# Kernel optimization log

Measured on AMD Instinct MI355X. Metric: run time of the kernel, lower is better.

Reference implementation:

```python
import jax, jax.numpy as jnp
import numpy as np

# MANO kinematic tree (16 LBS joints): wrist root, 5 fingers x 3 joints
PARENTS = np.array([-1, 0, 1, 2, 0, 4, 5, 0, 7, 8, 0, 10, 11, 0, 13, 14])
B, NV, NJ_LBS, NJ_REG, NCOMPS = 4096, 1084, 16, 21, 45


def rodrigues(r):
    """Axis-angle [N,3] -> rotation matrices [N,3,3]."""
    eps = 1e-8
    angle = jnp.sqrt(jnp.sum(r * r, axis=-1, keepdims=True) + eps)  # [N,1]
    axis = r / angle
    c = jnp.cos(angle)[..., None]  # [N,1,1]
    s = jnp.sin(angle)[..., None]
    x, y, z = axis[:, 0], axis[:, 1], axis[:, 2]
    zeros = jnp.zeros_like(x)
    K = jnp.stack([zeros, -z, y, z, zeros, -x, -y, x, zeros], axis=-1).reshape(-1, 3, 3)
    I = jnp.eye(3, dtype=r.dtype)
    return I + s * K + (1.0 - c) * jnp.matmul(K, K)


def global_rigid_transform(Rs, Js):
    """Rs [B,16,3,3], Js [B,16,3] -> (posed joints [B,16,3], relative transforms A [B,16,4,4])."""
    b = Rs.shape[0]
    bottom = jnp.broadcast_to(jnp.array([0.0, 0.0, 0.0, 1.0], dtype=Rs.dtype), (b, 1, 4))

    def make_A(R, t):  # R [B,3,3], t [B,3] -> [B,4,4]
        top = jnp.concatenate([R, t[..., None]], axis=-1)
        return jnp.concatenate([top, bottom], axis=1)

    results = [make_A(Rs[:, 0], Js[:, 0])]
    for i in range(1, NJ_LBS):  # fixed small loop over kinematic tree
        p = int(PARENTS[i])
        t = Js[:, i] - Js[:, p]
        results.append(jnp.matmul(results[p], make_A(Rs[:, i], t)))
    A_world = jnp.stack(results, axis=1)  # [B,16,4,4]
    new_J = A_world[:, :, :3, 3]
    # A = A_world - pack(A_world @ [J;0])  (remove rest-pose joint translation)
    Jh = jnp.concatenate([Js, jnp.zeros_like(Js[..., :1])], axis=-1)  # [B,16,4]
    init_bone = jnp.einsum('bjpq,bjq->bjp', A_world, Jh)  # [B,16,4]
    A_rel = A_world.at[:, :, :, 3].add(-init_bone)
    return new_J, A_rel


def setup_inputs() -> dict:
    key = jax.random.key(0)
    ks = jax.random.split(key, 8)
    beta = jax.random.normal(ks[0], (B, 10), dtype=jnp.float32)
    theta = jax.random.normal(ks[1], (B, NCOMPS), dtype=jnp.float32)
    wrist_euler = jax.random.normal(ks[2], (B, 3), dtype=jnp.float32) * 0.3
    v_template = jax.random.normal(ks[3], (NV, 3), dtype=jnp.float32) * 0.1
    J_regressor = jax.nn.softmax(jax.random.normal(ks[4], (NV, NJ_REG), dtype=jnp.float32) * 4.0, axis=0)
    hands_comp = jax.random.normal(ks[5], (NCOMPS, 45), dtype=jnp.float32) * 0.05
    hands_mean = jax.random.normal(ks[6], (45,), dtype=jnp.float32) * 0.1
    weights = jax.nn.softmax(jax.random.normal(ks[7], (NV, NJ_LBS), dtype=jnp.float32) * 4.0, axis=1)
    return {"beta": beta, "theta": theta, "wrist_euler": wrist_euler,
            "v_template": v_template, "J_regressor": J_regressor,
            "hands_comp": hands_comp, "hands_mean": hands_mean, "weights": weights}


def reference(beta, theta, wrist_euler, v_template, J_regressor, hands_comp, hands_mean, weights):
    num_batch = beta.shape[0]  # beta only sets batch; forward ignores its values (as in source)
    # rest-pose joints from template: [21,3]
    Jt = jnp.einsum('vc,vj->jc', v_template, J_regressor)
    J = jnp.broadcast_to(Jt[None], (num_batch, NJ_REG, 3))
    # pose_type == 'pca'
    euler_pose = theta @ hands_comp + hands_mean  # [B,45]
    Rs = rodrigues(euler_pose.reshape(-1, 3)).reshape(num_batch, 15, 3, 3)
    global_rot = rodrigues(wrist_euler.reshape(-1, 3)).reshape(num_batch, 1, 3, 3)
    R_all = jnp.concatenate([global_rot, Rs], axis=1)  # [B,16,3,3]
    J_transformed, A = global_rigid_transform(R_all, J[:, :NJ_LBS])
    # linear blend skinning: T = W @ A  -> [B,Nv,4,4]
    W = jnp.broadcast_to(weights[None], (num_batch, NV, NJ_LBS))
    T = jnp.matmul(W, A.reshape(num_batch, NJ_LBS, 16)).reshape(num_batch, NV, 4, 4)
    vh = jnp.concatenate([v_template, jnp.ones_like(v_template[:, :1])], axis=-1)  # [Nv,4]
    verts = jnp.einsum('bvpq,vq->bvp', T, vh)[:, :, :3]  # [B,Nv,3]
    joints = jnp.einsum('bvc,vj->bjc', verts, J_regressor)  # [B,21,3]
    return verts, joints
```

## Files before the change

### kernel.cpp

```cpp
#include <hip/hip_runtime.h>

#define NV 1084
#define NVPAD 1088
#define NPART 64
#define NBATCH 8

typedef __attribute__((ext_vector_type(8))) short short8v;
typedef __attribute__((ext_vector_type(4))) float f32x4;

__device__ inline unsigned short f2bf(float f) {
    unsigned int u = __float_as_uint(f);
    unsigned int r = (u + 0x7FFFu + ((u >> 16) & 1u)) >> 16;
    return (unsigned short)r;
}


__device__ inline void rodrigues9(float x, float y, float z, float R[9]) {
    float n2 = x * x + y * y + z * z + 1e-8f;
    float angle = sqrtf(n2);
    float inv = 1.0f / angle;
    float ax = x * inv, ay = y * inv, az = z * inv;
    float c = cosf(angle), s = sinf(angle);
    float C = 1.0f - c;
    R[0] = 1.0f - C * (ay * ay + az * az);
    R[1] = -s * az + C * ax * ay;
    R[2] = s * ay + C * ax * az;
    R[3] = s * az + C * ax * ay;
    R[4] = 1.0f - C * (ax * ax + az * az);
    R[5] = -s * ax + C * ay * az;
    R[6] = -s * ay + C * ax * az;
    R[7] = s * ax + C * ay * az;
    R[8] = 1.0f - C * (ax * ax + ay * ay);
}

__global__ __launch_bounds__(384) void prep_kernel(
    const float* __restrict__ vt, const float* __restrict__ jreg,
    const float* __restrict__ wts, float* __restrict__ Mpart,
    unsigned short* __restrict__ Gbf) {
    int blk = blockIdx.x;
    int t = threadIdx.x;
    if (blk < NPART) {
        int p = blk;
        int v0 = p * 17, v1 = min(v0 + 17, NV);
        float* mp = Mpart + (size_t)p * 1392;
        if (t < 336) {
            int j = t >> 4, k = t & 15;
            float m0 = 0.f, m1 = 0.f, m2 = 0.f, s = 0.f;
            for (int v = v0; v < v1; ++v) {
                float jw = jreg[v * 21 + j] * wts[v * 16 + k];
                m0 += jw * vt[v * 3 + 0];
                m1 += jw * vt[v * 3 + 1];
                m2 += jw * vt[v * 3 + 2];
                s += jw;
            }
            mp[t * 4 + 0] = m0;
            mp[t * 4 + 1] = m1;
            mp[t * 4 + 2] = m2;
            mp[t * 4 + 3] = s;
        } else if (t < 384) {
            int o = t - 336;
            int j = o / 3, c = o - j * 3;
            float acc = 0.f;
            for (int v = v0; v < v1; ++v) acc += vt[v * 3 + c] * jreg[v * 21 + j];
            mp[1344 + o] = acc;
        }
    } else {
        int idx = (blk - NPART) * 384 + t;
        if (idx < NVPAD * 64) {
            int v = idx >> 6, i = idx & 63;
            int k = i >> 2, d = i & 3;
            float val = 0.f;
            if (v < NV) {
                float vh = (d == 3) ? 1.f : vt[v * 3 + d];
                val = wts[v * 16 + k] * vh;
            }
            Gbf[idx] = f2bf(val);
        }
    }
}

__global__ __launch_bounds__(256) void fk_kernel(
    const float* __restrict__ theta, const float* __restrict__ wrist,
    const float* __restrict__ hc, const float* __restrict__ hm,
    const float* __restrict__ Mpart, float* __restrict__ wsA,
    float* __restrict__ Mfinal, unsigned short* __restrict__ Abf,
    int total, int nFK) {
    int blk = blockIdx.x;
    int t = threadIdx.x;
    if (blk >= nFK) {
        __shared__ float sm[256];
        int q = (blk - nFK) * 64 + (t & 63);
        int pg = t >> 6;
        float acc = 0.f;
#pragma unroll
        for (int u = 0; u < 16; ++u) acc += Mpart[(size_t)(pg * 16 + u) * 1392 + q];
        sm[t] = acc;
        __syncthreads();
        if (pg == 0) Mfinal[q] = sm[t] + sm[t + 64] + sm[t + 128] + sm[t + 192];
        return;
    }
    __shared__ float sred[192];
    __shared__ float sj[48];
    if (t < 192) {
        int g = t / 48, o = t - g * 48;
        float acc = 0.f;
#pragma unroll
        for (int u = 0; u < 16; ++u)
            acc += Mpart[(size_t)(g * 16 + u) * 1392 + 1344 + o];
        sred[t] = acc;
    }
    __syncthreads();
    if (t < 48) sj[t] = sred[t] + sred[48 + t] + sred[96 + t] + sred[144 + t];
    __syncthreads();

    int idx = blk * 256 + t;
    if (idx >= total) return;
    int b = idx / 5, r = idx - b * 5;

    float e[9];
    {
        const float* th = theta + (size_t)b * 45;
        int base = 9 * r;
#pragma unroll
        for (int col = 0; col < 9; ++col) e[col] = hm[base + col];
        for (int k = 0; k < 45; ++k) {
            float tk = th[k];
            const float* hck = hc + k * 45 + base;
#pragma unroll
            for (int col = 0; col < 9; ++col) e[col] += tk * hck[col];
        }
    }

    float R[9];
    rodrigues9(wrist[b * 3 + 0], wrist[b * 3 + 1], wrist[b * 3 + 2], R);
    float J0x = sj[0], J0y = sj[1], J0z = sj[2];
    float Ap[12];
    Ap[0] = R[0]; Ap[1] = R[1]; Ap[2] = R[2]; Ap[3] = J0x;
    Ap[4] = R[3]; Ap[5] = R[4]; Ap[6] = R[5]; Ap[7] = J0y;
    Ap[8] = R[6]; Ap[9] = R[7]; Ap[10] = R[8]; Ap[11] = J0z;
    float* out = wsA + (size_t)b * 192;
    if (r == 0) {
#pragma unroll
        for (int row = 0; row < 3; ++row) {
            float a0 = Ap[row * 4 + 0], a1 = Ap[row * 4 + 1], a2 = Ap[row * 4 + 2];
            float a3 = Ap[row * 4 + 3] - (a0 * J0x + a1 * J0y + a2 * J0z);
            out[row * 4 + 0] = a0;
            out[row * 4 + 1] = a1;
            out[row * 4 + 2] = a2;
            out[row * 4 + 3] = a3;
            ushort4 h;
            h.x = f2bf(a0); h.y = f2bf(a1); h.z = f2bf(a2); h.w = f2bf(a3);
            *(ushort4*)(Abf + (size_t)(3 * b + row) * 64) = h;
        }
    }
    float px = J0x, py = J0y, pz = J0z;
#pragma unroll
    for (int s = 0; s < 3; ++s) {
        int i = r * 3 + s + 1;
        rodrigues9(e[3 * s + 0], e[3 * s + 1], e[3 * s + 2], R);
        float jx = sj[i * 3 + 0], jy = sj[i * 3 + 1], jz = sj[i * 3 + 2];
        float tx = jx - px, ty = jy - py, tz = jz - pz;
        float An[12];
#pragma unroll
        for (int row = 0; row < 3; ++row) {
            An[row * 4 + 0] = Ap[row * 4 + 0] * R[0] + Ap[row * 4 + 1] * R[3] + Ap[row * 4 + 2] * R[6];
            An[row * 4 + 1] = Ap[row * 4 + 0] * R[1] + Ap[row * 4 + 1] * R[4] + Ap[row * 4 + 2] * R[7];
            An[row * 4 + 2] = Ap[row * 4 + 0] * R[2] + Ap[row * 4 + 1] * R[5] + Ap[row * 4 + 2] * R[8];
            An[row * 4 + 3] = Ap[row * 4 + 3] + Ap[row * 4 + 0] * tx + Ap[row * 4 + 1] * ty + Ap[row * 4 + 2] * tz;
        }
        float* oi = out + i * 12;
#pragma unroll
        for (int row = 0; row < 3; ++row) {
            float a0 = An[row * 4 + 0], a1 = An[row * 4 + 1], a2 = An[row * 4 + 2];
            float a3 = An[row * 4 + 3] - (a0 * jx + a1 * jy + a2 * jz);
            oi[row * 4 + 0] = a0;
            oi[row * 4 + 1] = a1;
            oi[row * 4 + 2] = a2;
            oi[row * 4 + 3] = a3;
            ushort4 h;
            h.x = f2bf(a0); h.y = f2bf(a1); h.z = f2bf(a2); h.w = f2bf(a3);
            *(ushort4*)(Abf + (size_t)(3 * b + row) * 64 + 4 * i) = h;
        }
#pragma unroll
        for (int q = 0; q < 12; ++q) Ap[q] = An[q];
        px = jx; py = jy; pz = jz;
    }
}

#define SCW 1092
__global__ __launch_bounds__(256) void verts_joints_kernel(
    const float* __restrict__ wsA, const float* __restrict__ Mfinal,
    const unsigned short* __restrict__ Abf, const unsigned short* __restrict__ Gbf,
    float* __restrict__ verts, float* __restrict__ jout, int nVB) {
    int bid = blockIdx.x;
    int t = threadIdx.x;

    if (bid < nVB) {
        __shared__ float sC[12 * SCW];
        int b0 = bid * 4;
        int w = t >> 6, lane = t & 63;
        int lrow = lane & 15, lk = lane >> 4;

        const unsigned short* Ar = Abf + (size_t)(b0 * 3 + lrow) * 64 + lk * 8;
        short8v a0 = *(const short8v*)Ar;
        short8v a1 = *(const short8v*)(Ar + 32);

        for (int vt4 = w; vt4 < NVPAD / 16; vt4 += 4) {
            int v = vt4 * 16 + lrow;
            const unsigned short* Br = Gbf + (size_t)v * 64 + lk * 8;
            short8v g0 = *(const short8v*)Br;
            short8v g1 = *(const short8v*)(Br + 32);
            f32x4 acc = {0.f, 0.f, 0.f, 0.f};
            acc = __builtin_amdgcn_mfma_f32_16x16x32_bf16(a0, g0, acc, 0, 0, 0);
            acc = __builtin_amdgcn_mfma_f32_16x16x32_bf16(a1, g1, acc, 0, 0, 0);
            if (lk < 3) {
                float* dst = &sC[(lk * 4) * SCW + vt4 * 16 + lrow];
#pragma unroll
                for (int q = 0; q < 4; ++q) dst[q * SCW] = acc[q];
            }
        }
        __syncthreads();

        float* outp = verts + (size_t)b0 * (NV * 3);
#pragma unroll 1
        for (int f = t; f < 3252; f += 256) {
            int bl = f / 813;
            int off = (f - bl * 813) * 4;
            f32x4 val;
#pragma unroll
            for (int j = 0; j < 4; ++j) {
                int o = off + j;
                int v_ = o / 3, p_ = o - v_ * 3;
                val[j] = sC[(bl * 3 + p_) * SCW + v_];
            }
            __builtin_nontemporal_store(val, (f32x4*)(outp + (size_t)f * 4));
        }
    } else {
        int b0 = (bid - nVB) * NBATCH;
        for (int o = t; o < NBATCH * 63; o += 256) {
            int bl = o / 63;
            int rem = o - bl * 63;
            int j = rem / 3;
            int c = rem - j * 3;
            const float* A = wsA + (size_t)(b0 + bl) * 192 + c * 4;
            const float* Mj = Mfinal + j * 64;
            float acc = 0.f;
#pragma unroll
            for (int k = 0; k < 16; ++k) {
                float4 av = *(const float4*)&A[k * 12];
                float4 m = *(const float4*)&Mj[k * 4];
                acc += av.x * m.x + av.y * m.y + av.z * m.z + av.w * m.w;
            }
            __builtin_nontemporal_store(acc, jout + (size_t)(b0 + bl) * 63 + rem);
        }
    }
}

extern "C" void kernel_launch(void* const* d_in, const int* in_sizes, int n_in,
                              void* d_out, int out_size, void* d_ws, size_t ws_size,
                              hipStream_t stream) {
    const float* theta = (const float*)d_in[1];
    const float* wrist = (const float*)d_in[2];
    const float* vtpl  = (const float*)d_in[3];
    const float* jreg  = (const float*)d_in[4];
    const float* hc    = (const float*)d_in[5];
    const float* hm    = (const float*)d_in[6];
    const float* wts   = (const float*)d_in[7];
    int B = in_sizes[1] / 45;

    float* ws     = (float*)d_ws;
    float* wsA    = ws;
    float* Mpart  = ws + (size_t)B * 192;
    float* Mfinal = Mpart + (size_t)NPART * 1392;
    unsigned short* Gbf = (unsigned short*)(Mfinal + 1344);
    unsigned short* Abf = Gbf + (size_t)NVPAD * 64;
    float* verts  = (float*)d_out;
    float* jout   = verts + (size_t)B * NV * 3;

    int nG = (NVPAD * 64 + 383) / 384;
    prep_kernel<<<NPART + nG, 384, 0, stream>>>(vtpl, jreg, wts, Mpart, Gbf);
    int nFK = (B * 5 + 255) / 256;
    fk_kernel<<<nFK + 21, 256, 0, stream>>>(theta, wrist, hc, hm, Mpart, wsA,
                                            Mfinal, Abf, B * 5, nFK);
    int nVB = B / 4;
    verts_joints_kernel<<<nVB + B / NBATCH, 256, 0, stream>>>(
        wsA, Mfinal, Abf, Gbf, verts, jout, nVB);
}
```

Baseline: 51.84 us.

## Fuse prep and FK kernels, compute regressor reductions in-block instead of partials

After: 74.08 us. +42.9%, slower.

```diff
diff --git a/kernel.cpp b/kernel.cpp
--- a/kernel.cpp
+++ b/kernel.cpp
@@ -2,7 +2,6 @@
 
 #define NV 1084
 #define NVPAD 1088
-#define NPART 64
 #define NBATCH 8
 
 typedef __attribute__((ext_vector_type(8))) short short8v;
@@ -33,39 +32,18 @@
     R[8] = 1.0f - C * (ax * ax + ay * ay);
 }
 
-__global__ __launch_bounds__(384) void prep_kernel(
+__global__ __launch_bounds__(256) void prep_fk_kernel(
+    const float* __restrict__ theta, const float* __restrict__ wrist,
+    const float* __restrict__ hc, const float* __restrict__ hm,
     const float* __restrict__ vt, const float* __restrict__ jreg,
-    const float* __restrict__ wts, float* __restrict__ Mpart,
-    unsigned short* __restrict__ Gbf) {
+    const float* __restrict__ wts, float* __restrict__ wsA,
+    float* __restrict__ Mfinal, unsigned short* __restrict__ Gbf,
+    unsigned short* __restrict__ Abf, int total, int nFK) {
     int blk = blockIdx.x;
     int t = threadIdx.x;
-    if (blk < NPART) {
-        int p = blk;
-        int v0 = p * 17, v1 = min(v0 + 17, NV);
-        float* mp = Mpart + (size_t)p * 1392;
-        if (t < 336) {
-            int j = t >> 4, k = t & 15;
-            float m0 = 0.f, m1 = 0.f, m2 = 0.f, s = 0.f;
-            for (int v = v0; v < v1; ++v) {
-                float jw = jreg[v * 21 + j] * wts[v * 16 + k];
-                m0 += jw * vt[v * 3 + 0];
-                m1 += jw * vt[v * 3 + 1];
-                m2 += jw * vt[v * 3 + 2];
-                s += jw;
-            }
-            mp[t * 4 + 0] = m0;
-            mp[t * 4 + 1] = m1;
-            mp[t * 4 + 2] = m2;
-            mp[t * 4 + 3] = s;
-        } else if (t < 384) {
-            int o = t - 336;
-            int j = o / 3, c = o - j * 3;
-            float acc = 0.f;
-            for (int v = v0; v < v1; ++v) acc += vt[v * 3 + c] * jreg[v * 21 + j];
-            mp[1344 + o] = acc;
-        }
-    } else {
-        int idx = (blk - NPART) * 384 + t;
+
+    if (blk >= nFK + 21) {
+        int idx = (blk - nFK - 21) * 256 + t;
         if (idx < NVPAD * 64) {
             int v = idx >> 6, i = idx & 63;
             int k = i >> 2, d = i & 3;
@@ -76,41 +54,39 @@
             }
             Gbf[idx] = f2bf(val);
         }
-    }
-}
-
-__global__ __launch_bounds__(256) void fk_kernel(
-    const float* __restrict__ theta, const float* __restrict__ wrist,
-    const float* __restrict__ hc, const float* __restrict__ hm,
-    const float* __restrict__ Mpart, float* __restrict__ wsA,
-    float* __restrict__ Mfinal, unsigned short* __restrict__ Abf,
-    int total, int nFK) {
-    int blk = blockIdx.x;
-    int t = threadIdx.x;
+        return;
+    }
     if (blk >= nFK) {
         __shared__ float sm[256];
         int q = (blk - nFK) * 64 + (t & 63);
-        int pg = t >> 6;
+        int vg = t >> 6;
+        int j = q >> 6;
+        int k = (q >> 2) & 15;
+        int d = q & 3;
+        int v0 = vg * 271, v1 = min(v0 + 271, NV);
         float acc = 0.f;
-#pragma unroll
-        for (int u = 0; u < 16; ++u) acc += Mpart[(size_t)(pg * 16 + u) * 1392 + q];
+        for (int v = v0; v < v1; ++v) {
+            float vh = (d == 3) ? 1.f : vt[v * 3 + d];
+            acc += jreg[v * 21 + j] * wts[v * 16 + k] * vh;
+        }
         sm[t] = acc;
         __syncthreads();
-        if (pg == 0) Mfinal[q] = sm[t] + sm[t + 64] + sm[t + 128] + sm[t + 192];
+        if (vg == 0) Mfinal[q] = sm[t] + sm[t + 64] + sm[t + 128] + sm[t + 192];
         return;
     }
-    __shared__ float sred[192];
+
+    __shared__ float sred[240];
     __shared__ float sj[48];
-    if (t < 192) {
+    if (t < 240) {
         int g = t / 48, o = t - g * 48;
+        int j = o / 3, c = o - j * 3;
+        int v0 = g * 217, v1 = min(v0 + 217, NV);
         float acc = 0.f;
-#pragma unroll
-        for (int u = 0; u < 16; ++u)
-            acc += Mpart[(size_t)(g * 16 + u) * 1392 + 1344 + o];
+        for (int v = v0; v < v1; ++v) acc += vt[v * 3 + c] * jreg[v * 21 + j];
         sred[t] = acc;
     }
     __syncthreads();
-    if (t < 48) sj[t] = sred[t] + sred[48 + t] + sred[96 + t] + sred[144 + t];
+    if (t < 48) sj[t] = sred[t] + sred[48 + t] + sred[96 + t] + sred[144 + t] + sred[192 + t];
     __syncthreads();
 
     int idx = blk * 256 + t;
@@ -270,18 +246,16 @@
 
     float* ws     = (float*)d_ws;
     float* wsA    = ws;
-    float* Mpart  = ws + (size_t)B * 192;
-    float* Mfinal = Mpart + (size_t)NPART * 1392;
+    float* Mfinal = ws + (size_t)B * 192;
     unsigned short* Gbf = (unsigned short*)(Mfinal + 1344);
     unsigned short* Abf = Gbf + (size_t)NVPAD * 64;
     float* verts  = (float*)d_out;
     float* jout   = verts + (size_t)B * NV * 3;
 
-    int nG = (NVPAD * 64 + 383) / 384;
-    prep_kernel<<<NPART + nG, 384, 0, stream>>>(vtpl, jreg, wts, Mpart, Gbf);
     int nFK = (B * 5 + 255) / 256;
-    fk_kernel<<<nFK + 21, 256, 0, stream>>>(theta, wrist, hc, hm, Mpart, wsA,
-                                            Mfinal, Abf, B * 5, nFK);
+    int nG = (NVPAD * 64 + 255) / 256;
+    prep_fk_kernel<<<nFK + 21 + nG, 256, 0, stream>>>(
+        theta, wrist, hc, hm, vtpl, jreg, wts, wsA, Mfinal, Gbf, Abf, B * 5, nFK);
     int nVB = B / 4;
     verts_joints_kernel<<<nVB + B / NBATCH, 256, 0, stream>>>(
         wsA, Mfinal, Abf, Gbf, verts, jout, nVB);
```
